# Optimization experiments

Hardware: AMD Instinct MI355X
Metric: run time of the kernel (lower is better)

The kernel has to match this reference:

```python
import jax, jax.numpy as jnp
import numpy as np

N_NODES = 50000
N_HYPEREDGES = 20000
N_EDGES = 1000000
N_RELATIONS = 256
IN_DIM = 128
OUT_DIM = 128
SEM_IN_DIM = 64
LN_EPS = 1e-5
LRELU_SLOPE = 0.01


def setup_inputs() -> dict:
    key = jax.random.key(0)
    ks = jax.random.split(key, 12)
    node_embeddings = jax.random.normal(ks[0], (N_NODES, IN_DIM), dtype=jnp.float32)
    semalink_embeddings = jax.random.normal(ks[1], (N_RELATIONS, SEM_IN_DIM), dtype=jnp.float32)
    hyperedge_embeddings = jax.random.normal(ks[2], (N_HYPEREDGES, IN_DIM), dtype=jnp.float32)
    # semalinks: (node_idx, hyperedge_idx, relation_idx) triples
    node_idx = jax.random.randint(ks[3], (N_EDGES,), 0, N_NODES)
    edge_idx = jax.random.randint(ks[4], (N_EDGES,), 0, N_HYPEREDGES)
    rel_idx = jax.random.randint(ks[5], (N_EDGES,), 0, N_RELATIONS)
    semalinks = jnp.stack([node_idx, edge_idx, rel_idx], axis=1).astype(jnp.int64)
    # parameters (xavier-like init scale)
    W_r = jax.random.normal(ks[6], (IN_DIM, OUT_DIM), dtype=jnp.float32) * (1.0 / np.sqrt(IN_DIM))
    lin_w = jax.random.normal(ks[7], (OUT_DIM, IN_DIM), dtype=jnp.float32) * (1.0 / np.sqrt(IN_DIM))
    lin_b = jnp.zeros((OUT_DIM,), dtype=jnp.float32)
    sem_w = jax.random.normal(ks[8], (OUT_DIM, SEM_IN_DIM), dtype=jnp.float32) * (1.0 / np.sqrt(SEM_IN_DIM))
    sem_b = jnp.zeros((OUT_DIM,), dtype=jnp.float32)
    ln_gamma = jnp.ones((OUT_DIM,), dtype=jnp.float32)
    ln_beta = jnp.zeros((OUT_DIM,), dtype=jnp.float32)
    return {
        "node_embeddings": node_embeddings,
        "semalink_embeddings": semalink_embeddings,
        "hyperedge_embeddings": hyperedge_embeddings,
        "W_r": W_r,
        "lin_w": lin_w,
        "lin_b": lin_b,
        "sem_w": sem_w,
        "sem_b": sem_b,
        "ln_gamma": ln_gamma,
        "ln_beta": ln_beta,
        "semalinks": semalinks,
    }


def reference(node_embeddings, semalink_embeddings, hyperedge_embeddings,
              W_r, lin_w, lin_b, sem_w, sem_b, ln_gamma, ln_beta, semalinks):
    H = hyperedge_embeddings.shape[0]
    node_idx = semalinks[:, 0]
    edge_idx = semalinks[:, 1]
    rel_idx = semalinks[:, 2]

    # semalink_linear
    sem_t = semalink_embeddings @ sem_w.T + sem_b          # [R, D]
    # projections through W_r (project once per node/hyperedge, then gather)
    r_mul_h_all = node_embeddings @ W_r                     # [N, D]
    r_mul_t_all = hyperedge_embeddings @ W_r                # [H, D]

    r_mul_h = r_mul_h_all[node_idx]                         # [E, D]
    t = jnp.tanh(r_mul_t_all[edge_idx] + sem_t[rel_idx])    # [E, D]
    scores = jnp.sum(r_mul_h * t, axis=-1)                  # [E]

    # segment softmax over hyperedge groups
    seg_max = jax.ops.segment_max(scores, edge_idx, num_segments=H)
    exp_s = jnp.exp(scores - seg_max[edge_idx])
    denom = jax.ops.segment_sum(exp_s, edge_idx, num_segments=H)
    alpha = exp_s / denom[edge_idx]                         # [E]

    # weighted sum of raw node embeddings per hyperedge (empty groups -> 0)
    agg = jax.ops.segment_sum(alpha[:, None] * node_embeddings[node_idx],
                              edge_idx, num_segments=H)     # [H, in_dim]

    out = agg @ lin_w.T + lin_b                             # [H, out_dim]
    out = jnp.where(out >= 0, out, LRELU_SLOPE * out)       # LeakyReLU
    # LayerNorm over last dim
    mu = jnp.mean(out, axis=-1, keepdims=True)
    var = jnp.mean(jnp.square(out - mu), axis=-1, keepdims=True)
    out = (out - mu) * jax.lax.rsqrt(var + LN_EPS) * ln_gamma + ln_beta
    # dropout: identity in eval mode
    return out
```

## Files before the change

### kernel.cpp

```cpp
#include <hip/hip_runtime.h>
#include <hip/hip_bf16.h>
#include <hip/hip_fp16.h>
#include <math.h>

#define N_NODES 50000
#define N_HYPER 20000
#define N_EDGES_C 1000000
#define N_REL 256
#define DIM 128
#define SEM_DIM 64
#define CAP 128

typedef unsigned int uint;
typedef unsigned short ushort;
typedef _Float16 v2h __attribute__((ext_vector_type(2)));
typedef _Float16 f16x8 __attribute__((ext_vector_type(8)));
typedef float f32x4 __attribute__((ext_vector_type(4)));

#define SC_2L2E 2.8853900817779268f
#define SC_L2E  1.4426950408889634f

__device__ inline ushort f16rn(float f) { return __half_as_ushort(__float2half_rn(f)); }
__device__ inline __half2 u2h2(uint u) { return __builtin_bit_cast(__half2, u); }

__device__ inline float fdot2(__half2 a, __half2 b, float c) {
#if __has_builtin(__builtin_amdgcn_fdot2)
  return __builtin_amdgcn_fdot2(__builtin_bit_cast(v2h, a),
                                __builtin_bit_cast(v2h, b), c, false);
#else
  float2 fa = __half22float2(a), fb = __half22float2(b);
  return fmaf(fa.x, fb.x, fmaf(fa.y, fb.y, c));
#endif
}

__global__ __launch_bounds__(256) void k_prep(const float* __restrict__ Wr,
                                              const float* __restrict__ linw,
                                              ushort* __restrict__ WT_h,
                                              ushort* __restrict__ LW_h) {
  int i = blockIdx.x * 256 + threadIdx.x;
  if (i < DIM * DIM) {
    int k = i >> 7, c = i & 127;
    WT_h[c * DIM + k] = f16rn(Wr[i]);
  } else if (i < 2 * DIM * DIM) {
    int j = i - DIM * DIM;
    LW_h[j] = f16rn(linw[j]);
  }
}

__global__ __launch_bounds__(128) void k_sem(const float* __restrict__ emb,
                                             const float* __restrict__ sem_w,
                                             const float* __restrict__ sem_b,
                                             ushort* __restrict__ sem_t_h) {
  __shared__ float sW[DIM][SEM_DIM + 1];
  __shared__ float sE[SEM_DIM];
  int t = threadIdx.x;
  for (int i = t; i < DIM * SEM_DIM; i += 128) sW[i / SEM_DIM][i % SEM_DIM] = sem_w[i];
  int r = blockIdx.x;
  if (t < SEM_DIM) sE[t] = emb[r * SEM_DIM + t];
  __syncthreads();
  float acc = sem_b[t];
#pragma unroll 8
  for (int k = 0; k < SEM_DIM; ++k) acc = fmaf(sE[k], sW[t][k], acc);
  sem_t_h[r * DIM + t] = f16rn(acc * SC_2L2E);
}

template <bool EMIT_NE>
__global__ __launch_bounds__(256) void k_mfma(const float* __restrict__ X,
                                              const ushort* __restrict__ B0h,
                                              ushort* __restrict__ C0,
                                              ushort* __restrict__ ne_h,
                                              float scale0, int M) {
  __shared__ uint sA[64 * 64];
  __shared__ uint sB0[128 * 64];
  int t = threadIdx.x;
  int bm = blockIdx.x * 64;
  int rows = min(64, M - bm);
  for (int ch = t; ch < 64 * 16; ch += 256) {
    int r = ch >> 4, c0 = ch & 15;
    uint4 v = {0u, 0u, 0u, 0u};
    if (r < rows) {
      const float4* gp = (const float4*)(X + (size_t)(bm + r) * DIM + c0 * 8);
      float4 x0 = gp[0], x1 = gp[1];
      v.x = (uint)f16rn(x0.x) | ((uint)f16rn(x0.y) << 16);
      v.y = (uint)f16rn(x0.z) | ((uint)f16rn(x0.w) << 16);
      v.z = (uint)f16rn(x1.x) | ((uint)f16rn(x1.y) << 16);
      v.w = (uint)f16rn(x1.z) | ((uint)f16rn(x1.w) << 16);
    }
    *(uint4*)&sA[r * 64 + ((c0 ^ (r & 15)) << 2)] = v;
  }
  for (int ch = t; ch < 128 * 16; ch += 256) {
    int c = ch >> 4, c0 = ch & 15;
    uint4 v = *(const uint4*)(B0h + c * DIM + c0 * 8);
    *(uint4*)&sB0[c * 64 + ((c0 ^ (c & 15)) << 2)] = v;
  }
  __syncthreads();
  int wid = t >> 6, lane = t & 63;
  int arow = (wid << 4) + (lane & 15);
  int kg = lane >> 4;
  int cl = lane & 15;
  f32x4 acc0[8];
#pragma unroll
  for (int nt = 0; nt < 8; ++nt) acc0[nt] = (f32x4){0.f, 0.f, 0.f, 0.f};
#pragma unroll
  for (int ks = 0; ks < 4; ++ks) {
    int chA = (ks << 2) + kg;
    f16x8 afrag = *(const f16x8*)&sA[arow * 64 + ((chA ^ (arow & 15)) << 2)];
#pragma unroll
    for (int nt = 0; nt < 8; ++nt) {
      int col = (nt << 4) + cl;
      f16x8 b0 = *(const f16x8*)&sB0[col * 64 + ((chA ^ (col & 15)) << 2)];
      acc0[nt] = __builtin_amdgcn_mfma_f32_16x16x32_f16(afrag, b0, acc0[nt], 0, 0, 0);
    }
  }
  int rbase = (wid << 4) + (kg << 2);
#pragma unroll
  for (int nt = 0; nt < 8; ++nt) {
#pragma unroll
    for (int r = 0; r < 4; ++r) {
      int row = rbase + r;
      if (row < rows)
        C0[(size_t)(bm + row) * DIM + (nt << 4) + cl] = f16rn(acc0[nt][r] * scale0);
    }
  }
  if (EMIT_NE) {
    for (int ch = t; ch < 64 * 16; ch += 256) {
      int r = ch >> 4, c0 = ch & 15;
      if (r < rows) {
        uint4 v = *(uint4*)&sA[r * 64 + ((c0 ^ (r & 15)) << 2)];
        *(uint4*)(ne_h + (size_t)(bm + r) * DIM + c0 * 8) = v;
      }
    }
  }
}

__global__ __launch_bounds__(256) void k_scatter(const int* __restrict__ sl,
                                                 int* __restrict__ cnt,
                                                 uint* __restrict__ ed) {
  int i = blockIdx.x * 256 + threadIdx.x;
  int e0 = i * 4;
  if (e0 >= N_EDGES_C) return;
  const int4* p = (const int4*)(sl + 3 * e0);
  int4 a = p[0], b = p[1], c = p[2];
  int nd[4] = {a.x, a.w, b.z, c.y};
  int hh[4] = {a.y, b.x, b.w, c.z};
  int rl[4] = {a.z, b.y, c.x, c.w};
#pragma unroll
  for (int j = 0; j < 4; ++j) {
    int pos = atomicAdd(&cnt[hh[j]], 1);
    if (pos < CAP) ed[(size_t)hh[j] * CAP + pos] = (uint)nd[j] | ((uint)rl[j] << 16);
  }
}

#define NG 8
#define BLK_H 2
__global__ __launch_bounds__(128) void k_agg(
    const ushort* __restrict__ rh_h, const ushort* __restrict__ rt_h,
    const ushort* __restrict__ semt_h, const ushort* __restrict__ ne_h,
    const uint* __restrict__ ed, const int* __restrict__ cnt,
    ushort* __restrict__ agg_h) {
  int wave = threadIdx.x >> 6;
  int lane = threadIdx.x & 63;
  int h = blockIdx.x * BLK_H + wave;
  int g = lane >> 3;
  int pos = lane & 7;
  int d0 = pos * 16;
  const uint4* tp = (const uint4*)(rt_h + ((size_t)h << 7) + d0);
  uint4 tba = tp[0], tbb = tp[1];
  __half2 tb0 = u2h2(tba.x), tb1 = u2h2(tba.y), tb2 = u2h2(tba.z), tb3 = u2h2(tba.w);
  __half2 tb4 = u2h2(tbb.x), tb5 = u2h2(tbb.y), tb6 = u2h2(tbb.z), tb7 = u2h2(tbb.w);
  const __half2 one2 = __floats2half2_rn(1.0f, 1.0f);
  const __half2 m2 = __floats2half2_rn(-2.0f, -2.0f);
  size_t base = (size_t)h * CAP;
  int n = min(cnt[h], CAP);
  float l = 0.0f;
  float4 a0 = {0,0,0,0}, a1 = {0,0,0,0}, a2 = {0,0,0,0}, a3 = {0,0,0,0};

  for (int e = g; e < n; e += NG) {
    uint q = ed[base + e];
    int node = (int)(q & 0xffffu);
    int rel = (int)(q >> 16);
    const uint4* hp = (const uint4*)(rh_h + ((size_t)node << 7) + d0);
    const uint4* sp = (const uint4*)(semt_h + ((size_t)rel << 7) + d0);
    const uint4* np = (const uint4*)(ne_h + ((size_t)node << 7) + d0);
    uint4 ha = hp[0], hb = hp[1];
    uint4 sa = sp[0], sb = sp[1];
    uint4 na = np[0], nb = np[1];
    float da = 0.0f, db = 0.0f;
#define TP(US, UH, TB, ACC)                      \
    {                                            \
      __half2 arg = __hadd2(TB, u2h2(US));       \
      __half2 e2v = h2exp2(arg);                 \
      __half2 r2 = h2rcp(__hadd2(e2v, one2));    \
      __half2 t2 = __hfma2(m2, r2, one2);        \
      ACC = fdot2(u2h2(UH), t2, ACC);            \
    }
    TP(sa.x, ha.x, tb0, da) TP(sa.y, ha.y, tb1, db)
    TP(sa.z, ha.z, tb2, da) TP(sa.w, ha.w, tb3, db)
    TP(sb.x, hb.x, tb4, da) TP(sb.y, hb.y, tb5, db)
    TP(sb.z, hb.z, tb6, da) TP(sb.w, hb.w, tb7, db)
#undef TP
    float dot = da + db;
    dot += __shfl_xor(dot, 1, 64);
    dot += __shfl_xor(dot, 2, 64);
    dot += __shfl_xor(dot, 4, 64);
    float p = exp2f(dot);
    l += p;
    float2 n0 = __half22float2(u2h2(na.x));
    float2 n1 = __half22float2(u2h2(na.y));
    float2 n2 = __half22float2(u2h2(na.z));
    float2 n3 = __half22float2(u2h2(na.w));
    float2 n4 = __half22float2(u2h2(nb.x));
    float2 n5 = __half22float2(u2h2(nb.y));
    float2 n6 = __half22float2(u2h2(nb.z));
    float2 n7 = __half22float2(u2h2(nb.w));
    a0.x = fmaf(p, n0.x, a0.x); a0.y = fmaf(p, n0.y, a0.y);
    a0.z = fmaf(p, n1.x, a0.z); a0.w = fmaf(p, n1.y, a0.w);
    a1.x = fmaf(p, n2.x, a1.x); a1.y = fmaf(p, n2.y, a1.y);
    a1.z = fmaf(p, n3.x, a1.z); a1.w = fmaf(p, n3.y, a1.w);
    a2.x = fmaf(p, n4.x, a2.x); a2.y = fmaf(p, n4.y, a2.y);
    a2.z = fmaf(p, n5.x, a2.z); a2.w = fmaf(p, n5.y, a2.w);
    a3.x = fmaf(p, n6.x, a3.x); a3.y = fmaf(p, n6.y, a3.y);
    a3.z = fmaf(p, n7.x, a3.z); a3.w = fmaf(p, n7.y, a3.w);
  }
#pragma unroll
  for (int mo = 8; mo < 64; mo <<= 1) {
    l += __shfl_xor(l, mo, 64);
    a0.x += __shfl_xor(a0.x, mo, 64); a0.y += __shfl_xor(a0.y, mo, 64);
    a0.z += __shfl_xor(a0.z, mo, 64); a0.w += __shfl_xor(a0.w, mo, 64);
    a1.x += __shfl_xor(a1.x, mo, 64); a1.y += __shfl_xor(a1.y, mo, 64);
    a1.z += __shfl_xor(a1.z, mo, 64); a1.w += __shfl_xor(a1.w, mo, 64);
    a2.x += __shfl_xor(a2.x, mo, 64); a2.y += __shfl_xor(a2.y, mo, 64);
    a2.z += __shfl_xor(a2.z, mo, 64); a2.w += __shfl_xor(a2.w, mo, 64);
    a3.x += __shfl_xor(a3.x, mo, 64); a3.y += __shfl_xor(a3.y, mo, 64);
    a3.z += __shfl_xor(a3.z, mo, 64); a3.w += __shfl_xor(a3.w, mo, 64);
  }
  if (g == 0) {
    float inv = (l > 0.0f) ? __builtin_amdgcn_rcpf(l) : 0.0f;
    uint4 w0, w1;
    w0.x = (uint)f16rn(a0.x * inv) | ((uint)f16rn(a0.y * inv) << 16);
    w0.y = (uint)f16rn(a0.z * inv) | ((uint)f16rn(a0.w * inv) << 16);
    w0.z = (uint)f16rn(a1.x * inv) | ((uint)f16rn(a1.y * inv) << 16);
    w0.w = (uint)f16rn(a1.z * inv) | ((uint)f16rn(a1.w * inv) << 16);
    w1.x = (uint)f16rn(a2.x * inv) | ((uint)f16rn(a2.y * inv) << 16);
    w1.y = (uint)f16rn(a2.z * inv) | ((uint)f16rn(a2.w * inv) << 16);
    w1.z = (uint)f16rn(a3.x * inv) | ((uint)f16rn(a3.y * inv) << 16);
    w1.w = (uint)f16rn(a3.z * inv) | ((uint)f16rn(a3.w * inv) << 16);
    *(uint4*)(agg_h + ((size_t)h << 7) + d0) = w0;
    *(uint4*)(agg_h + ((size_t)h << 7) + d0 + 8) = w1;
  }
}

__global__ __launch_bounds__(256) void k_mfma_ln(
    const ushort* __restrict__ Ah, const ushort* __restrict__ LWh,
    const float* __restrict__ bias, const float* __restrict__ gamma,
    const float* __restrict__ beta, float* __restrict__ out, int M) {
  __shared__ uint sA[64 * 64];
  __shared__ uint sB0[128 * 64];
  int t = threadIdx.x;
  int bm = blockIdx.x * 64;
  int rows = min(64, M - bm);
  for (int ch = t; ch < 64 * 16; ch += 256) {
    int r = ch >> 4, c0 = ch & 15;
    uint4 v = {0u, 0u, 0u, 0u};
    if (r < rows) v = *(const uint4*)(Ah + (size_t)(bm + r) * DIM + c0 * 8);
    *(uint4*)&sA[r * 64 + ((c0 ^ (r & 15)) << 2)] = v;
  }
  for (int ch = t; ch < 128 * 16; ch += 256) {
    int c = ch >> 4, c0 = ch & 15;
    uint4 v = *(const uint4*)(LWh + c * DIM + c0 * 8);
    *(uint4*)&sB0[c * 64 + ((c0 ^ (c & 15)) << 2)] = v;
  }
  __syncthreads();
  int wid = t >> 6, lane = t & 63;
  int arow = (wid << 4) + (lane & 15);
  int kg = lane >> 4;
  int cl = lane & 15;
  f32x4 acc0[8];
#pragma unroll
  for (int nt = 0; nt < 8; ++nt) acc0[nt] = (f32x4){0.f, 0.f, 0.f, 0.f};
#pragma unroll
  for (int ks = 0; ks < 4; ++ks) {
    int chA = (ks << 2) + kg;
    f16x8 afrag = *(const f16x8*)&sA[arow * 64 + ((chA ^ (arow & 15)) << 2)];
#pragma unroll
    for (int nt = 0; nt < 8; ++nt) {
      int col = (nt << 4) + cl;
      f16x8 b0 = *(const f16x8*)&sB0[col * 64 + ((chA ^ (col & 15)) << 2)];
      acc0[nt] = __builtin_amdgcn_mfma_f32_16x16x32_f16(afrag, b0, acc0[nt], 0, 0, 0);
    }
  }
  float bv[8], gv[8], ev[8];
#pragma unroll
  for (int nt = 0; nt < 8; ++nt) {
    int col = (nt << 4) + cl;
    bv[nt] = bias[col]; gv[nt] = gamma[col]; ev[nt] = beta[col];
  }
  int rbase = (wid << 4) + (kg << 2);
#pragma unroll
  for (int r = 0; r < 4; ++r) {
    float s = 0.f, q = 0.f;
#pragma unroll
    for (int nt = 0; nt < 8; ++nt) {
      float x = acc0[nt][r] + bv[nt];
      x = x >= 0.0f ? x : 0.01f * x;
      acc0[nt][r] = x;
      s += x; q += x * x;
    }
#pragma unroll
    for (int mo = 1; mo < 16; mo <<= 1) {
      s += __shfl_xor(s, mo, 64);
      q += __shfl_xor(q, mo, 64);
    }
    float mu = s * (1.0f / 128.0f);
    float var = q * (1.0f / 128.0f) - mu * mu;
    float inv = rsqrtf(var + 1e-5f);
    int row = rbase + r;
    if (row < rows) {
      float* Or = out + (size_t)(bm + row) * DIM;
#pragma unroll
      for (int nt = 0; nt < 8; ++nt)
        Or[(nt << 4) + cl] = (acc0[nt][r] - mu) * inv * gv[nt] + ev[nt];
    }
  }
}

extern "C" void kernel_launch(void* const* d_in, const int* in_sizes, int n_in,
                              void* d_out, int out_size, void* d_ws, size_t ws_size,
                              hipStream_t stream) {
  const float* node_emb = (const float*)d_in[0];
  const float* sem_emb = (const float*)d_in[1];
  const float* hyper_emb = (const float*)d_in[2];
  const float* W_r = (const float*)d_in[3];
  const float* lin_w = (const float*)d_in[4];
  const float* lin_b = (const float*)d_in[5];
  const float* sem_w = (const float*)d_in[6];
  const float* sem_b = (const float*)d_in[7];
  const float* ln_g = (const float*)d_in[8];
  const float* ln_b = (const float*)d_in[9];
  const int* sl = (const int*)d_in[10];
  float* out = (float*)d_out;

  char* ws = (char*)d_ws;
  ushort* agg_h = (ushort*)ws;
  int* cnt = (int*)(ws + 5120000);
  uint* ed = (uint*)(ws + 5201920);
  ushort* rt_h = (ushort*)(ws + 15441920);
  ushort* rh_h = (ushort*)(ws + 20561920);
  ushort* ne_h = (ushort*)(ws + 33361920);
  ushort* semt_h = (ushort*)(ws + 46161920);
  ushort* WT_h = (ushort*)(ws + 46227456);
  ushort* LW_h = (ushort*)(ws + 46260224);

  hipMemsetAsync(cnt, 0, sizeof(int) * 20480, stream);
  k_prep<<<(2 * DIM * DIM + 255) / 256, 256, 0, stream>>>(W_r, lin_w, WT_h, LW_h);
  k_sem<<<N_REL, 128, 0, stream>>>(sem_emb, sem_w, sem_b, semt_h);
  k_mfma<false><<<(N_HYPER + 63) / 64, 256, 0, stream>>>(
      hyper_emb, WT_h, rt_h, nullptr, SC_2L2E, N_HYPER);
  k_mfma<true><<<(N_NODES + 63) / 64, 256, 0, stream>>>(
      node_emb, WT_h, rh_h, ne_h, SC_L2E, N_NODES);
  k_scatter<<<(N_EDGES_C / 4 + 255) / 256, 256, 0, stream>>>(sl, cnt, ed);
  k_agg<<<N_HYPER / BLK_H, 128, 0, stream>>>(rh_h, rt_h, semt_h, ne_h, ed, cnt, agg_h);
  k_mfma_ln<<<(N_HYPER + 63) / 64, 256, 0, stream>>>(
      agg_h, LW_h, lin_b, ln_g, ln_b, out, N_HYPER);
}
```

Baseline: 255.9 us.

## Merge prep/projection kernels and software-pipeline edge gathers in aggregation

Fuses the weight-prep and semantic-linear kernels into one launch, and the hyperedge and node projection GEMMs into one launch, cutting launch count and tail effects. In the aggregation kernel, each wave preloads its hyperedge's edge list into registers and distributes entries via shuffles. It also prefetches the next round's gathered rows while computing the current one, to hide gather latency. This raises register pressure and adds masked extra iterations.

```diff
diff --git a/kernel.cpp b/kernel.cpp
--- a/kernel.cpp
+++ b/kernel.cpp
@@ -33,47 +33,56 @@
 #endif
 }
 
-__global__ __launch_bounds__(256) void k_prep(const float* __restrict__ Wr,
-                                              const float* __restrict__ linw,
-                                              ushort* __restrict__ WT_h,
-                                              ushort* __restrict__ LW_h) {
-  int i = blockIdx.x * 256 + threadIdx.x;
-  if (i < DIM * DIM) {
-    int k = i >> 7, c = i & 127;
-    WT_h[c * DIM + k] = f16rn(Wr[i]);
-  } else if (i < 2 * DIM * DIM) {
-    int j = i - DIM * DIM;
-    LW_h[j] = f16rn(linw[j]);
-  }
-}
-
-__global__ __launch_bounds__(128) void k_sem(const float* __restrict__ emb,
-                                             const float* __restrict__ sem_w,
-                                             const float* __restrict__ sem_b,
-                                             ushort* __restrict__ sem_t_h) {
-  __shared__ float sW[DIM][SEM_DIM + 1];
-  __shared__ float sE[SEM_DIM];
+__device__ inline uint getq(uint qv0, uint qv1, int src) {
+  uint a = __shfl(qv0, src & 63, 64);
+  uint b = __shfl(qv1, src & 63, 64);
+  return (src < 64) ? a : b;
+}
+
+__global__ __launch_bounds__(128) void k_pre(
+    const float* __restrict__ emb, const float* __restrict__ sem_w,
+    const float* __restrict__ sem_b, ushort* __restrict__ sem_t_h,
+    const float* __restrict__ Wr, const float* __restrict__ linw,
+    ushort* __restrict__ WT_h, ushort* __restrict__ LW_h) {
+  int b = blockIdx.x;
   int t = threadIdx.x;
-  for (int i = t; i < DIM * SEM_DIM; i += 128) sW[i / SEM_DIM][i % SEM_DIM] = sem_w[i];
-  int r = blockIdx.x;
-  if (t < SEM_DIM) sE[t] = emb[r * SEM_DIM + t];
-  __syncthreads();
-  float acc = sem_b[t];
+  if (b < N_REL) {
+    __shared__ float sW[DIM][SEM_DIM + 1];
+    __shared__ float sE[SEM_DIM];
+    for (int i = t; i < DIM * SEM_DIM; i += 128) sW[i / SEM_DIM][i % SEM_DIM] = sem_w[i];
+    if (t < SEM_DIM) sE[t] = emb[b * SEM_DIM + t];
+    __syncthreads();
+    float acc = sem_b[t];
 #pragma unroll 8
-  for (int k = 0; k < SEM_DIM; ++k) acc = fmaf(sE[k], sW[t][k], acc);
-  sem_t_h[r * DIM + t] = f16rn(acc * SC_2L2E);
-}
-
-template <bool EMIT_NE>
-__global__ __launch_bounds__(256) void k_mfma(const float* __restrict__ X,
-                                              const ushort* __restrict__ B0h,
-                                              ushort* __restrict__ C0,
-                                              ushort* __restrict__ ne_h,
-                                              float scale0, int M) {
+    for (int k = 0; k < SEM_DIM; ++k) acc = fmaf(sE[k], sW[t][k], acc);
+    sem_t_h[b * DIM + t] = f16rn(acc * SC_2L2E);
+  } else {
+    int i = (b - N_REL) * 128 + t;
+    if (i < DIM * DIM) {
+      int k = i >> 7, c = i & 127;
+      WT_h[c * DIM + k] = f16rn(Wr[i]);
+    } else {
+      int j = i - DIM * DIM;
+      LW_h[j] = f16rn(linw[j]);
+    }
+  }
+}
+
+__global__ __launch_bounds__(256) void k_mfma_all(
+    const float* __restrict__ hyper_emb, const float* __restrict__ node_emb,
+    const ushort* __restrict__ WT_h, ushort* __restrict__ rt_h,
+    ushort* __restrict__ rh_h, ushort* __restrict__ ne_h) {
+  const int HB = (N_HYPER + 63) / 64;
   __shared__ uint sA[64 * 64];
   __shared__ uint sB0[128 * 64];
+  int b = blockIdx.x;
+  bool isH = b < HB;
+  const float* X = isH ? hyper_emb : node_emb;
+  int bm = (isH ? b : b - HB) * 64;
+  int M = isH ? N_HYPER : N_NODES;
+  ushort* C0 = isH ? rt_h : rh_h;
+  float scale0 = isH ? SC_2L2E : SC_L2E;
   int t = threadIdx.x;
-  int bm = blockIdx.x * 64;
   int rows = min(64, M - bm);
   for (int ch = t; ch < 64 * 16; ch += 256) {
     int r = ch >> 4, c0 = ch & 15;
@@ -90,7 +99,7 @@
   }
   for (int ch = t; ch < 128 * 16; ch += 256) {
     int c = ch >> 4, c0 = ch & 15;
-    uint4 v = *(const uint4*)(B0h + c * DIM + c0 * 8);
+    uint4 v = *(const uint4*)(WT_h + c * DIM + c0 * 8);
     *(uint4*)&sB0[c * 64 + ((c0 ^ (c & 15)) << 2)] = v;
   }
   __syncthreads();
@@ -122,7 +131,7 @@
         C0[(size_t)(bm + row) * DIM + (nt << 4) + cl] = f16rn(acc0[nt][r] * scale0);
     }
   }
-  if (EMIT_NE) {
+  if (!isH) {
     for (int ch = t; ch < 64 * 16; ch += 256) {
       int r = ch >> 4, c0 = ch & 15;
       if (r < rows) {
@@ -172,19 +181,31 @@
   const __half2 m2 = __floats2half2_rn(-2.0f, -2.0f);
   size_t base = (size_t)h * CAP;
   int n = min(cnt[h], CAP);
+  uint qv0 = (lane < n) ? ed[base + lane] : 0u;
+  uint qv1 = (64 + lane < n) ? ed[base + 64 + lane] : 0u;
+  int rounds = (n + NG - 1) / NG;
   float l = 0.0f;
   float4 a0 = {0,0,0,0}, a1 = {0,0,0,0}, a2 = {0,0,0,0}, a3 = {0,0,0,0};
-
-  for (int e = g; e < n; e += NG) {
-    uint q = ed[base + e];
-    int node = (int)(q & 0xffffu);
-    int rel = (int)(q >> 16);
+  uint4 ha, hb, sa, sb, na, nb;
+  if (rounds > 0) {
+    uint q = getq(qv0, qv1, g);
+    int node = (int)(q & 0xffffu), rel = (int)(q >> 16);
     const uint4* hp = (const uint4*)(rh_h + ((size_t)node << 7) + d0);
     const uint4* sp = (const uint4*)(semt_h + ((size_t)rel << 7) + d0);
     const uint4* np = (const uint4*)(ne_h + ((size_t)node << 7) + d0);
-    uint4 ha = hp[0], hb = hp[1];
-    uint4 sa = sp[0], sb = sp[1];
-    uint4 na = np[0], nb = np[1];
+    ha = hp[0]; hb = hp[1]; sa = sp[0]; sb = sp[1]; na = np[0]; nb = np[1];
+  }
+  for (int r = 0; r < rounds; ++r) {
+    uint4 pha, phb, psa, psb, pna, pnb;
+    bool pf = (r + 1) < rounds;
+    if (pf) {
+      uint qn = getq(qv0, qv1, (r + 1) * NG + g);
+      int node = (int)(qn & 0xffffu), rel = (int)(qn >> 16);
+      const uint4* hp = (const uint4*)(rh_h + ((size_t)node << 7) + d0);
+      const uint4* sp = (const uint4*)(semt_h + ((size_t)rel << 7) + d0);
+      const uint4* np = (const uint4*)(ne_h + ((size_t)node << 7) + d0);
+      pha = hp[0]; phb = hp[1]; psa = sp[0]; psb = sp[1]; pna = np[0]; pnb = np[1];
+    }
     float da = 0.0f, db = 0.0f;
 #define TP(US, UH, TB, ACC)                      \
     {                                            \
@@ -203,7 +224,7 @@
     dot += __shfl_xor(dot, 1, 64);
     dot += __shfl_xor(dot, 2, 64);
     dot += __shfl_xor(dot, 4, 64);
-    float p = exp2f(dot);
+    float p = (g + r * NG < n) ? exp2f(dot) : 0.0f;
     l += p;
     float2 n0 = __half22float2(u2h2(na.x));
     float2 n1 = __half22float2(u2h2(na.y));
@@ -221,6 +242,7 @@
     a2.z = fmaf(p, n5.x, a2.z); a2.w = fmaf(p, n5.y, a2.w);
     a3.x = fmaf(p, n6.x, a3.x); a3.y = fmaf(p, n6.y, a3.y);
     a3.z = fmaf(p, n7.x, a3.z); a3.w = fmaf(p, n7.y, a3.w);
+    if (pf) { ha = pha; hb = phb; sa = psa; sb = psb; na = pna; nb = pnb; }
   }
 #pragma unroll
   for (int mo = 8; mo < 64; mo <<= 1) {
@@ -351,15 +373,14 @@
   ushort* WT_h = (ushort*)(ws + 46227456);
   ushort* LW_h = (ushort*)(ws + 46260224);
 
+  const int HB = (N_HYPER + 63) / 64;
+  const int NB = (N_NODES + 63) / 64;
   hipMemsetAsync(cnt, 0, sizeof(int) * 20480, stream);
-  k_prep<<<(2 * DIM * DIM + 255) / 256, 256, 0, stream>>>(W_r, lin_w, WT_h, LW_h);
-  k_sem<<<N_REL, 128, 0, stream>>>(sem_emb, sem_w, sem_b, semt_h);
-  k_mfma<false><<<(N_HYPER + 63) / 64, 256, 0, stream>>>(
-      hyper_emb, WT_h, rt_h, nullptr, SC_2L2E, N_HYPER);
-  k_mfma<true><<<(N_NODES + 63) / 64, 256, 0, stream>>>(
-      node_emb, WT_h, rh_h, ne_h, SC_L2E, N_NODES);
+  k_pre<<<N_REL + 256, 128, 0, stream>>>(sem_emb, sem_w, sem_b, semt_h,
+                                         W_r, lin_w, WT_h, LW_h);
   k_scatter<<<(N_EDGES_C / 4 + 255) / 256, 256, 0, stream>>>(sl, cnt, ed);
+  k_mfma_all<<<HB + NB, 256, 0, stream>>>(hyper_emb, node_emb, WT_h,
+                                          rt_h, rh_h, ne_h);
   k_agg<<<N_HYPER / BLK_H, 128, 0, stream>>>(rh_h, rt_h, semt_h, ne_h, ed, cnt, agg_h);
-  k_mfma_ln<<<(N_HYPER + 63) / 64, 256, 0, stream>>>(
-      agg_h, LW_h, lin_b, ln_g, ln_b, out, N_HYPER);
-}
+  k_mfma_ln<<<HB, 256, 0, stream>>>(agg_h, LW_h, lin_b, ln_g, ln_b, out, N_HYPER);
+}
```

After: 248.1 us. -3.1%, faster.
